# Kernel tuning notes

Hardware: AMD Instinct MI355X
Metric: run time of the kernel (lower is better)

Reference implementation:

```python
import jax, jax.numpy as jnp
import numpy as np

SIZE = 128
WIN = SIZE // 4   # sliding-window size == region size (32)
HALF = WIN // 2   # 16


def _conv(x, w, pad, groups=1):
    return jax.lax.conv_general_dilated(x, w, (1, 1), [(pad, pad), (pad, pad)],
        dimension_numbers=('NCHW', 'OIHW', 'NCHW'), feature_group_count=groups)


def _resize(x, h, w):
    # F.interpolate(..., mode='bilinear', align_corners=False)
    return jax.image.resize(x, (x.shape[0], x.shape[1], h, w), 'bilinear', antialias=False)


def _gauss_kernels():
    ax = np.linspace(-2.0, 2.0, 5)
    xx, yy = np.meshgrid(ax, ax)
    g = np.exp(-(xx ** 2 + yy ** 2) / 2.0) / (2.0 * np.pi)  # sigma = 1
    gx = (-xx * g).astype(np.float32)
    gy = (-yy * g).astype(np.float32)
    return (jnp.asarray(np.tile(gx[None, None], (3, 3, 1, 1))),
            jnp.asarray(np.tile(gy[None, None], (3, 3, 1, 1))))


def _edge_extract(x):
    Gx, Gy = _gauss_kernels()
    h = _conv(x, Gx, 2)
    v = _conv(x, Gy, 2)
    return jnp.tanh(jnp.sqrt(h * h + v * v + 1e-8))


def _color_moments(x, win=5):
    # F.unfold-based local mean / unbiased var / skewness, via depthwise box sums
    C = x.shape[1]
    n = float(win * win)
    ones = jnp.ones((C, 1, win, win), x.dtype)
    box = lambda z: _conv(z, ones, win // 2, groups=C)
    s1 = box(x); s2 = box(x * x); s3 = box(x * x * x)
    mean = s1 / n
    var = (s2 - n * mean * mean) / (n - 1.0)               # unbiased, matches torch.var
    m3 = (s3 - 3.0 * mean * s2 + 2.0 * n * mean ** 3) / n  # E[(x-m)^3]
    skew = m3 / (jnp.sqrt(jnp.maximum(var, 0.0)) ** 3 + 1e-6)
    return jnp.concatenate([mean, var, skew], 1)


def _locate_region(c):
    # scipy: gradient magnitude < 0.2 -> 4-connected label at argmax -> bbox center
    H, W = c.shape
    flat = jnp.argmax(c)
    xm = (flat // W).astype(jnp.int32)
    ym = (flat % W).astype(jnp.int32)
    gm = jnp.hypot(jnp.gradient(c, axis=0), jnp.gradient(c, axis=1))
    mask = gm < 0.2
    seed = jnp.zeros((H, W), bool).at[xm, ym].set(True) & mask

    def dil(r):
        d = r
        d = d | jnp.pad(r[1:, :], ((0, 1), (0, 0)))
        d = d | jnp.pad(r[:-1, :], ((1, 0), (0, 0)))
        d = d | jnp.pad(r[:, 1:], ((0, 0), (0, 1)))
        d = d | jnp.pad(r[:, :-1], ((0, 0), (1, 0)))
        return d & mask

    def body(s):
        r, _ = s
        nr = dil(r)
        return (nr, jnp.any(nr != r))

    region, _ = jax.lax.while_loop(lambda s: s[1], body, (seed, jnp.any(seed)))
    rows = jnp.any(region, 1); cols = jnp.any(region, 0)
    rs = jnp.argmax(rows); re = H - jnp.argmax(rows[::-1])
    cs = jnp.argmax(cols); ce = W - jnp.argmax(cols[::-1])
    ok = mask[xm, ym]  # label_at_max != 0
    x1 = jnp.where(ok, ((rs + re) // 2).astype(jnp.int32), xm)
    y1 = jnp.where(ok, ((cs + ce) // 2).astype(jnp.int32), ym)
    return x1, y1


def _affine_grid(move, H, W):
    # theta = [[1,0,tx],[0,1,ty]] with (tx,ty)=move, align_corners=False
    bx = (2.0 * jnp.arange(W, dtype=jnp.float32) + 1.0) / W - 1.0
    by = (2.0 * jnp.arange(H, dtype=jnp.float32) + 1.0) / H - 1.0
    gx = bx[None, None, :] + move[:, 0, None, None]
    gy = by[None, :, None] + move[:, 1, None, None]
    return jnp.stack(jnp.broadcast_arrays(gx, gy), -1)  # [B,H,W,2]


def _grid_sample(x, grid):
    # bilinear, zeros padding, align_corners=False (torch defaults)
    B, C, H, W = x.shape
    ix = ((grid[..., 0] + 1.0) * W - 1.0) / 2.0
    iy = ((grid[..., 1] + 1.0) * H - 1.0) / 2.0
    ix0 = jnp.floor(ix).astype(jnp.int32)
    iy0 = jnp.floor(iy).astype(jnp.int32)
    wx1 = ix - ix0; wy1 = iy - iy0
    b = jnp.arange(B)[:, None, None]

    def g(yy, xx):
        valid = ((xx >= 0) & (xx < W) & (yy >= 0) & (yy < H)).astype(x.dtype)
        v = x[b, :, jnp.clip(yy, 0, H - 1), jnp.clip(xx, 0, W - 1)]  # [B,Hg,Wg,C]
        return v * valid[..., None]

    out = (g(iy0, ix0) * ((1 - wy1) * (1 - wx1))[..., None]
         + g(iy0, ix0 + 1) * ((1 - wy1) * wx1)[..., None]
         + g(iy0 + 1, ix0) * (wy1 * (1 - wx1))[..., None]
         + g(iy0 + 1, ix0 + 1) * (wy1 * wx1)[..., None])
    return jnp.transpose(out, (0, 3, 1, 2))


def _bn_relu6(x, w, b):
    # BatchNorm2d in training mode (batch stats, biased var, eps=1e-5) + ReLU6
    m = x.mean((0, 2, 3), keepdims=True)
    v = ((x - m) ** 2).mean((0, 2, 3), keepdims=True)
    y = (x - m) / jnp.sqrt(v + 1e-5) * w[None, :, None, None] + b[None, :, None, None]
    return jnp.clip(y, 0.0, 6.0)


def setup_inputs():
    key = jax.random.key(0)
    ks = jax.random.split(key, 8)
    B, C = 8, 64
    return dict(
        warm_flag=1,
        feat1=jax.random.normal(ks[0], (B, C, SIZE, SIZE), jnp.float32),
        feat2=jax.random.normal(ks[1], (B, C, SIZE, SIZE), jnp.float32),
        cam1=jax.random.uniform(ks[2], (B, 64, 64), jnp.float32),
        cam2=jax.random.uniform(ks[3], (B, 64, 64), jnp.float32),
        f_g=jax.random.uniform(ks[4], (B, 3, 512, 512), jnp.float32),
        f_e=jax.random.uniform(ks[5], (B, 3, 512, 512), jnp.float32),
        conv1_w=jax.random.normal(ks[6], (C, 3, 3, 3), jnp.float32) * 0.1,
        conv1_b=jnp.zeros((C,), jnp.float32),
        conv2_w=jax.random.normal(ks[7], (C, 9, 3, 3), jnp.float32) * 0.1,
        conv2_b=jnp.zeros((C,), jnp.float32),
        bn_w=jnp.ones((C,), jnp.float32),
        bn_b=jnp.zeros((C,), jnp.float32),
    )


def reference(warm_flag, feat1, feat2, cam1, cam2, f_g, f_e,
              conv1_w, conv1_b, conv2_w, conv2_b, bn_w, bn_b):
    B = cam1.shape[0]
    c1 = _resize(cam1[:, None], SIZE, SIZE)
    c2 = _resize(cam2[:, None], SIZE, SIZE)

    if warm_flag == 1:
        # numpy/scipy path in torch is detached from autograd
        c1s = jax.lax.stop_gradient(c1)
        c2s = jax.lax.stop_gradient(c2)
        x1, y1 = jax.vmap(_locate_region)(c1s[:, 0])
        # valid-mode box convolution of cam2 with ones((H//4, W//4)), argmax
        box = jax.lax.conv_general_dilated(c2s, jnp.ones((1, 1, WIN, WIN), c2.dtype), (1, 1),
            'VALID', dimension_numbers=('NCHW', 'OIHW', 'NCHW'))[:, 0]
        Wv = box.shape[-1]
        flat = jnp.argmax(box.reshape(B, -1), -1)
        x2 = (flat // Wv + HALF).astype(jnp.int32)
        y2 = (flat % Wv + HALF).astype(jnp.int32)

        idx = jnp.arange(SIZE)
        def rect(xc, yc):
            r = (idx[None, :] >= jnp.maximum(xc - HALF, 0)[:, None]) & \
                (idx[None, :] < jnp.minimum(xc + HALF, SIZE)[:, None])
            cc = (idx[None, :] >= jnp.maximum(yc - HALF, 0)[:, None]) & \
                 (idx[None, :] < jnp.minimum(yc + HALF, SIZE)[:, None])
            return r[:, None, :, None] & cc[:, None, None, :]
        mask1 = rect(x1, y1).astype(feat1.dtype)
        mask2 = rect(x2, y2).astype(feat2.dtype)
        mi1 = jnp.stack([x1, y1], -1).astype(jnp.float32)
        mi2 = jnp.stack([x2, y2], -1).astype(jnp.float32)
    else:
        mask1 = jnp.zeros_like(feat1)
        mask2 = jnp.zeros_like(feat2)
        mi1 = jnp.zeros((B, 2), jnp.float32)
        mi2 = jnp.zeros((B, 2), jnp.float32)

    cam2_move = (mi2 - mi1) / (SIZE // 2)
    cam1_move = (mi1 - mi2) / (SIZE // 2)
    grid1 = _affine_grid(cam1_move, SIZE, SIZE)
    grid2 = _affine_grid(cam2_move, SIZE, SIZE)

    moments = _resize(_color_moments(f_e), SIZE, SIZE)   # [B,9,128,128]
    edge = _resize(_edge_extract(f_g), SIZE, SIZE)       # [B,3,128,128]
    feat1_edge = jnp.clip(_conv(edge, conv1_w, 1) + conv1_b[None, :, None, None], 0.0, 6.0)
    feat2_color = _conv(moments, conv2_w, 1) + conv2_b[None, :, None, None]

    feat2_move = _grid_sample(feat2_color * mask2, grid2)
    feat1_edge_move = _grid_sample(feat1_edge * mask1, grid1)

    Bc, C, H, W = feat1.shape
    f1 = feat1.reshape(Bc, C, -1)
    f2 = feat2.reshape(Bc, C, -1)
    f2m = feat2_move.reshape(Bc, C, -1)
    f1m = feat1_edge_move.reshape(Bc, C, -1)

    f2_attn = jax.nn.softmax(jnp.einsum('bcn,bdn->bcd', f2m, f1), -1)  # [B,C,C]
    feat1_apply = jnp.einsum('bcd,bdn->bcn', f2_attn, f1).reshape(Bc, C, H, W)
    f1_attn = jax.nn.softmax(jnp.einsum('bcn,bdn->bcd', f1m, f2), -1)
    feat2_apply = jnp.einsum('bcd,bdn->bcn', f1_attn, f2).reshape(Bc, C, H, W)

    feat1_apply = _bn_relu6(feat1_apply, bn_w, bn_b)
    feat2_apply = _bn_relu6(feat2_apply, bn_w, bn_b)

    if warm_flag == 0:
        return (feat1, feat2, grid1, grid2, feat1_edge, feat2_color, f1_attn, f2_attn, feat1, feat2)
    return (feat1_apply, feat2_apply, grid1, grid2, feat1_edge, feat2_color, f1_attn, f2_attn, feat1, feat2)
```

## Files before the change

kernel.cpp:

```cpp
#include <hip/hip_runtime.h>
#include <math.h>

#define SIZE 128
#define WIN 32
#define HALF 16
#define B 8
#define C 64
#define N (SIZE*SIZE)
#define BCN 8388608
#define BV 97

#define O_APPLY1   0
#define O_APPLY2   8388608
#define O_GRID1    16777216
#define O_GRID2    17039360
#define O_EDGEF    17301504
#define O_COLORF   25690112
#define O_ATTN1    34078720
#define O_ATTN2    34111488
#define O_FEAT1    34144256
#define O_FEAT2    42532864

#define WS_BNP     0
#define WS_XY      361472
#define WS_MOM     361600
#define WS_EDGE    1541248
#define WS_BN      1737856

#define NEGINF (-3.402823466e+38f)

typedef unsigned __int128 u128;

__device__ __forceinline__ u128 hfill(u128 g, u128 m) {
  u128 p = m;
  g |= p & (g << 1);  p &= p << 1;
  g |= p & (g << 2);  p &= p << 2;
  g |= p & (g << 4);  p &= p << 4;
  g |= p & (g << 8);  p &= p << 8;
  g |= p & (g << 16); p &= p << 16;
  g |= p & (g << 32); p &= p << 32;
  g |= p & (g << 64);
  p = m;
  g |= p & (g >> 1);  p &= p >> 1;
  g |= p & (g >> 2);  p &= p >> 2;
  g |= p & (g >> 4);  p &= p >> 4;
  g |= p & (g >> 8);  p &= p >> 8;
  g |= p & (g >> 16); p &= p >> 16;
  g |= p & (g >> 32); p &= p >> 32;
  g |= p & (g >> 64);
  return g;
}

__global__ __launch_bounds__(256) void k_front(
    const float* __restrict__ cam1, const float* __restrict__ cam2,
    int* __restrict__ xy, float* __restrict__ g1, float* __restrict__ g2) {
  int b = blockIdx.x, tid = threadIdx.x;
  __shared__ float sc[N];
  __shared__ float sc2[N];
  __shared__ float sv[256]; __shared__ int si[256];
  __shared__ unsigned long long mask64[256];
  __shared__ int s_xm, s_ym, s_ok;
  __shared__ int s_x1, s_y1, s_x2, s_y2;

  const float* src1 = cam1 + b * 4096;
  const float* src2 = cam2 + b * 4096;

  float bv = NEGINF; int bi = 0;
  for (int k = 0; k < 64; ++k) {
    int pix = k * 256 + tid;
    int i = pix >> 7, j = pix & 127;
    float fy = fminf(fmaxf(0.5f * (float)i - 0.25f, 0.f), 63.f);
    float fx = fminf(fmaxf(0.5f * (float)j - 0.25f, 0.f), 63.f);
    int y0 = (int)fy; float ty = fy - (float)y0; int y1i = min(y0 + 1, 63);
    int x0 = (int)fx; float tx = fx - (float)x0; int x1i = min(x0 + 1, 63);
    float a00 = src1[y0 * 64 + x0],  a01 = src1[y0 * 64 + x1i];
    float a10 = src1[y1i * 64 + x0], a11 = src1[y1i * 64 + x1i];
    float v1 = (1.f - ty) * ((1.f - tx) * a00 + tx * a01)
             + ty * ((1.f - tx) * a10 + tx * a11);
    float c00 = src2[y0 * 64 + x0],  c01 = src2[y0 * 64 + x1i];
    float c10 = src2[y1i * 64 + x0], c11 = src2[y1i * 64 + x1i];
    float v2 = (1.f - ty) * ((1.f - tx) * c00 + tx * c01)
             + ty * ((1.f - tx) * c10 + tx * c11);
    sc[pix] = v1; sc2[pix] = v2;
    if (v1 > bv) { bv = v1; bi = pix; }
  }
  sv[tid] = bv; si[tid] = bi;
  __syncthreads();
  for (int s = 128; s; s >>= 1) {
    if (tid < s) {
      float ov = sv[tid + s]; int oi = si[tid + s];
      if (ov > sv[tid] || (ov == sv[tid] && oi < si[tid])) { sv[tid] = ov; si[tid] = oi; }
    }
    __syncthreads();
  }
  if (tid == 0) { s_xm = si[0] >> 7; s_ym = si[0] & 127; }
  __syncthreads();

  for (int k = 0; k < 64; ++k) {
    int pix = k * 256 + tid;
    int i = pix >> 7, j = pix & 127;
    float gx_, gy_;
    if (i == 0)        gx_ = sc[128 + j] - sc[j];
    else if (i == 127) gx_ = sc[127 * 128 + j] - sc[126 * 128 + j];
    else               gx_ = 0.5f * (sc[(i + 1) * 128 + j] - sc[(i - 1) * 128 + j]);
    if (j == 0)        gy_ = sc[i * 128 + 1] - sc[i * 128];
    else if (j == 127) gy_ = sc[i * 128 + 127] - sc[i * 128 + 126];
    else               gy_ = 0.5f * (sc[i * 128 + j + 1] - sc[i * 128 + j - 1]);
    bool pred = hypotf(gx_, gy_) < 0.2f;
    unsigned long long bal = __ballot(pred);
    if ((tid & 63) == 0) mask64[(i << 1) + (j >> 6)] = bal;
  }
  __syncthreads();
  if (tid == 0) {
    unsigned long long wdd = mask64[(s_xm << 1) + (s_ym >> 6)];
    s_ok = (int)((wdd >> (s_ym & 63)) & 1ull);
  }
  __syncthreads();

  if (tid < 64) {
    int l = tid;
    u128 m0 = ((u128)mask64[4 * l])     | ((u128)mask64[4 * l + 1] << 64);
    u128 m1 = ((u128)mask64[4 * l + 2]) | ((u128)mask64[4 * l + 3] << 64);
    u128 g0 = 0, g1v = 0;
    if (s_ok && (s_xm >> 1) == l) {
      if ((s_xm & 1) == 0) g0  = ((u128)1) << s_ym;
      else                 g1v = ((u128)1) << s_ym;
    }
    g0  = hfill(g0 & m0, m0);
    g1v = hfill(g1v & m1, m1);
    for (;;) {
      unsigned long long ulo = __shfl_up((unsigned long long)g1v, 1);
      unsigned long long uhi = __shfl_up((unsigned long long)(g1v >> 64), 1);
      u128 up = (l > 0) ? (((u128)ulo) | ((u128)uhi << 64)) : (u128)0;
      unsigned long long dlo = __shfl_down((unsigned long long)g0, 1);
      unsigned long long dhi = __shfl_down((unsigned long long)(g0 >> 64), 1);
      u128 dn = (l < 63) ? (((u128)dlo) | ((u128)dhi << 64)) : (u128)0;
      u128 n0 = hfill((g0 | up | g1v) & m0, m0);
      u128 n1 = hfill((g1v | n0 | dn) & m1, m1);
      bool chg = (n0 != g0) || (n1 != g1v);
      g0 = n0; g1v = n1;
      if (!__any(chg)) break;
    }
    unsigned long long be = __ballot(g0 != 0);
    unsigned long long bo = __ballot(g1v != 0);
    unsigned long long cl = (unsigned long long)(g0 | g1v);
    unsigned long long chh = (unsigned long long)((g0 | g1v) >> 64);
    for (int off = 32; off; off >>= 1) {
      cl  |= __shfl_xor(cl, off);
      chh |= __shfl_xor(chh, off);
    }
    if (l == 0) {
      int rs = 0, re = 0, cs = 0, ce = 0;
      if (be | bo) {
        int af = be ? (__ffsll(be) - 1) : 1000;
        int bf = bo ? (__ffsll(bo) - 1) : 1000;
        rs = min(af * 2, bf * 2 + 1);
        int al = be ? (63 - __clzll(be)) : -1000;
        int bl = bo ? (63 - __clzll(bo)) : -1000;
        re = max(al * 2, bl * 2 + 1) + 1;
        cs = cl ? (__ffsll(cl) - 1) : 64 + (__ffsll(chh) - 1);
        ce = chh ? 128 - __clzll(chh) : 64 - __clzll(cl);
      }
      int x1, y1;
      if (s_ok) { x1 = (rs + re) >> 1; y1 = (cs + ce) >> 1; }
      else      { x1 = s_xm;           y1 = s_ym; }
      xy[b] = x1; xy[8 + b] = y1; s_x1 = x1; s_y1 = y1;
    }
  }
  __syncthreads();

  for (int idx = tid; idx < BV * 128; idx += 256) {
    int rr = idx >> 7, cc = idx & 127;
    float acc = 0.f;
    #pragma unroll
    for (int dy = 0; dy < WIN; ++dy) acc += sc2[(rr + dy) * 128 + cc];
    sc[idx] = acc;
  }
  __syncthreads();

  bv = NEGINF; bi = 0;
  for (int p = tid; p < BV * BV; p += 256) {
    int rr = p / BV, cc = p % BV;
    float s = 0.f;
    #pragma unroll
    for (int dx = 0; dx < WIN; ++dx) s += sc[rr * 128 + cc + dx];
    if (s > bv) { bv = s; bi = p; }
  }
  sv[tid] = bv; si[tid] = bi;
  __syncthreads();
  for (int s = 128; s; s >>= 1) {
    if (tid < s) {
      float ov = sv[tid + s]; int oi = si[tid + s];
      if (ov > sv[tid] || (ov == sv[tid] && oi < si[tid])) { sv[tid] = ov; si[tid] = oi; }
    }
    __syncthreads();
  }
  if (tid == 0) {
    int x2 = si[0] / BV + HALF, y2 = si[0] % BV + HALF;
    xy[16 + b] = x2; xy[24 + b] = y2; s_x2 = x2; s_y2 = y2;
  }
  __syncthreads();

  float x1f = (float)s_x1, y1f = (float)s_y1;
  float x2f = (float)s_x2, y2f = (float)s_y2;
  float m1x = (x1f - x2f) / 64.f, m1y = (y1f - y2f) / 64.f;
  float* g1b = g1 + (size_t)b * N * 2;
  float* g2b = g2 + (size_t)b * N * 2;
  for (int k = 0; k < 64; ++k) {
    int pix = k * 256 + tid;
    int h = pix >> 7, w = pix & 127;
    float bx = (2.f * (float)w + 1.f) / 128.f - 1.f;
    float by = (2.f * (float)h + 1.f) / 128.f - 1.f;
    g1b[pix * 2]     = bx + m1x; g1b[pix * 2 + 1] = by + m1y;
    g2b[pix * 2]     = bx - m1x; g2b[pix * 2 + 1] = by - m1y;
  }
}

__global__ __launch_bounds__(256) void k_prep(const float* __restrict__ fe,
                                              const float* __restrict__ fg,
                                              float* __restrict__ mom,
                                              float* __restrict__ edge) {
  __shared__ float sx[66 * 66];
  int tid = threadIdx.x;
  if (blockIdx.x < 1536) {
    int blk = blockIdx.x;
    int tile = blk & 63, ch = (blk >> 6) % 3, b = blk / 192;
    int ti0 = (tile >> 3) * 16, tj0 = (tile & 7) * 16;
    const float* src = fe + (size_t)(b * 3 + ch) * 262144;
    int oy0 = 4 * ti0 - 1, ox0 = 4 * tj0 - 1;
    for (int l = tid; l < 66 * 66; l += 256) {
      int r = l / 66, cc = l % 66;
      int gy = oy0 + r, gx = ox0 + cc;
      sx[l] = (gy >= 0 && gy < 512 && gx >= 0 && gx < 512) ? src[gy * 512 + gx] : 0.f;
    }
    __syncthreads();
    int ii = tid >> 4, jj = tid & 15;
    int i = ti0 + ii, j = tj0 + jj;
    float s1a[6], s2a[6], s3a[6], s1b[6], s2b[6], s3b[6];
    #pragma unroll
    for (int t = 0; t < 6; ++t) {
      float a1 = 0, a2 = 0, a3 = 0, b1 = 0, b2 = 0, b3 = 0;
      int lx = 4 * jj + t;
      #pragma unroll
      for (int r = 0; r < 6; ++r) {
        float v = sx[(4 * ii + r) * 66 + lx];
        float v2 = v * v, v3 = v2 * v;
        if (r < 5) { a1 += v; a2 += v2; a3 += v3; }
        if (r > 0) { b1 += v; b2 += v2; b3 += v3; }
      }
      s1a[t] = a1; s2a[t] = a2; s3a[t] = a3;
      s1b[t] = b1; s2b[t] = b2; s3b[t] = b3;
    }
    float am = 0, av = 0, as = 0;
    #pragma unroll
    for (int py = 0; py < 2; ++py) {
      #pragma unroll
      for (int px = 0; px < 2; ++px) {
        float s1 = 0, s2 = 0, s3 = 0;
        #pragma unroll
        for (int t = 0; t < 5; ++t) {
          s1 += py ? s1b[px + t] : s1a[px + t];
          s2 += py ? s2b[px + t] : s2a[px + t];
          s3 += py ? s3b[px + t] : s3a[px + t];
        }
        float mean = s1 / 25.f;
        float var  = (s2 - 25.f * mean * mean) / 24.f;
        float m3   = (s3 - 3.f * mean * s2 + 50.f * mean * mean * mean) / 25.f;
        float sq   = sqrtf(fmaxf(var, 0.f));
        float skew = m3 / (sq * sq * sq + 1e-6f);
        am += mean; av += var; as += skew;
      }
    }
    int base = (b * 9 + ch) * N + i * 128 + j;
    mom[base]         = 0.25f * am;
    mom[base + 3 * N] = 0.25f * av;
    mom[base + 6 * N] = 0.25f * as;
  } else {
    int blk = blockIdx.x - 1536;
    int tile = blk & 63, b = blk >> 6;
    int ti0 = (tile >> 3) * 16, tj0 = (tile & 7) * 16;
    const float* s0 = fg + (size_t)b * 3 * 262144;
    int oy0 = 4 * ti0 - 1, ox0 = 4 * tj0 - 1;
    for (int l = tid; l < 66 * 66; l += 256) {
      int r = l / 66, cc = l % 66;
      int gy = oy0 + r, gx = ox0 + cc;
      float v = 0.f;
      if (gy >= 0 && gy < 512 && gx >= 0 && gx < 512) {
        int o = gy * 512 + gx;
        v = s0[o] + s0[262144 + o] + s0[524288 + o];
      }
      sx[l] = v;
    }
    __syncthreads();
    int ii = tid >> 4, jj = tid & 15;
    int i = ti0 + ii, j = tj0 + jj;
    const float INV2PI = 0.15915494309189535f;
    float wg[5], ug[5];
    #pragma unroll
    for (int t = 0; t < 5; ++t) {
      float a = (float)t - 2.f;
      float e = expf(-0.5f * a * a);
      wg[t] = e; ug[t] = -a * e;
    }
    float rAa[6], rAb[6], rBa[6], rBb[6];
    #pragma unroll
    for (int t = 0; t < 6; ++t) {
      float aa = 0, ab = 0, ba = 0, bb = 0;
      int lx = 4 * jj + t;
      #pragma unroll
      for (int r = 0; r < 6; ++r) {
        float v = sx[(4 * ii + r) * 66 + lx];
        if (r < 5) { aa += v * wg[r]; ba += v * ug[r]; }
        if (r > 0) { ab += v * wg[r - 1]; bb += v * ug[r - 1]; }
      }
      rAa[t] = aa; rAb[t] = ab; rBa[t] = ba; rBb[t] = bb;
    }
    float acc = 0.f;
    #pragma unroll
    for (int py = 0; py < 2; ++py) {
      #pragma unroll
      for (int px = 0; px < 2; ++px) {
        float h = 0, v = 0;
        #pragma unroll
        for (int t = 0; t < 5; ++t) {
          float A  = py ? rAb[px + t] : rAa[px + t];
          float Bw = py ? rBb[px + t] : rBa[px + t];
          h += A * ug[t];
          v += Bw * wg[t];
        }
        h *= INV2PI; v *= INV2PI;
        acc += tanhf(sqrtf(h * h + v * v + 1e-8f));
      }
    }
    edge[b * N + i * 128 + j] = 0.25f * acc;
  }
}

__global__ __launch_bounds__(256) void k_conv12(
    const float* __restrict__ edge, const float* __restrict__ w1,
    const float* __restrict__ b1, float* __restrict__ o4,
    const float* __restrict__ mom, const float* __restrict__ w2,
    const float* __restrict__ b2, float* __restrict__ o5) {
  __shared__ float tin[9 * 324];
  __shared__ float wsm[64 * 84];
  int b = blockIdx.x >> 6, tile = blockIdx.x & 63;
  int ti0 = (tile >> 3) * 16, tj0 = (tile & 7) * 16;
  int tid = threadIdx.x;
  int i = tid >> 4, j = tid & 15;
  if (blockIdx.y == 0) {
    for (int l = tid; l < 324; l += 256) {
      int r = l / 18, cc = l % 18;
      int gi = ti0 + r - 1, gj = tj0 + cc - 1;
      tin[l] = (gi >= 0 && gi < 128 && gj >= 0 && gj < 128) ? edge[b * N + gi * 128 + gj] : 0.f;
    }
    for (int l = tid; l < 64 * 12; l += 256) {
      int o = l / 12, t = l % 12;
      wsm[l] = (t < 9) ? (w1[o * 27 + t] + w1[o * 27 + 9 + t] + w1[o * 27 + 18 + t]) : 0.f;
    }
    __syncthreads();
    float win[12];
    #pragma unroll
    for (int dy = 0; dy < 3; ++dy)
      #pragma unroll
      for (int dx = 0; dx < 3; ++dx)
        win[dy * 3 + dx] = tin[(i + dy) * 18 + (j + dx)];
    win[9] = 0.f; win[10] = 0.f; win[11] = 0.f;
    float* o = o4 + (size_t)b * C * N + (ti0 + i) * 128 + tj0 + j;
    for (int oc = 0; oc < C; ++oc) {
      const float4* wr = (const float4*)(wsm + oc * 12);
      float acc = b1[oc];
      #pragma unroll
      for (int q = 0; q < 3; ++q) {
        float4 w4 = wr[q];
        acc += w4.x * win[4 * q] + w4.y * win[4 * q + 1]
             + w4.z * win[4 * q + 2] + w4.w * win[4 * q + 3];
      }
      o[oc * N] = fminf(fmaxf(acc, 0.f), 6.f);
    }
  } else {
    for (int l = tid; l < 9 * 324; l += 256) {
      int ic = l / 324, rem = l % 324, r = rem / 18, cc = rem % 18;
      int gi = ti0 + r - 1, gj = tj0 + cc - 1;
      tin[l] = (gi >= 0 && gi < 128 && gj >= 0 && gj < 128) ? mom[(b * 9 + ic) * N + gi * 128 + gj] : 0.f;
    }
    for (int l = tid; l < 64 * 84; l += 256) {
      int o = l / 84, t = l % 84;
      wsm[l] = (t < 81) ? w2[o * 81 + t] : 0.f;
    }
    __syncthreads();
    float win[84];
    #pragma unroll
    for (int ic = 0; ic < 9; ++ic)
      #pragma unroll
      for (int dy = 0; dy < 3; ++dy)
        #pragma unroll
        for (int dx = 0; dx < 3; ++dx)
          win[ic * 9 + dy * 3 + dx] = tin[ic * 324 + (i + dy) * 18 + (j + dx)];
    win[81] = 0.f; win[82] = 0.f; win[83] = 0.f;
    float* o = o5 + (size_t)b * C * N + (ti0 + i) * 128 + tj0 + j;
    for (int oc = 0; oc < C; ++oc) {
      const float4* wr = (const float4*)(wsm + oc * 84);
      float acc = b2[oc];
      #pragma unroll
      for (int q = 0; q < 21; ++q) {
        float4 w4 = wr[q];
        acc += w4.x * win[4 * q] + w4.y * win[4 * q + 1]
             + w4.z * win[4 * q + 2] + w4.w * win[4 * q + 3];
      }
      o[oc * N] = acc;
    }
  }
}

__global__ __launch_bounds__(256) void k_logits(const float* __restrict__ aB1,
                                                const float* __restrict__ bB1,
                                                const float* __restrict__ aB2,
                                                const float* __restrict__ bB2,
                                                float* __restrict__ lg,
                                                const int* __restrict__ xy) {
  int mode = blockIdx.y;
  const float* aBase = mode ? aB2 : aB1;
  const float* bBase = mode ? bB2 : bB1;
  int b = blockIdx.x >> 4, sl = blockIdx.x & 15;
  int tid = threadIdx.x;
  int ci = (tid >> 4) << 2, di = (tid & 15) << 2;
  float* o = lg + (size_t)(((mode * 8 + b) * 16 + sl)) * 4096;

  int x1 = xy[b], y1 = xy[8 + b], x2 = xy[16 + b], y2 = xy[24 + b];
  int dyh, dxw, rlo, rhi, clo, chi;
  if (mode == 0) {
    dyh = y1 - y2; dxw = x1 - x2;
    rlo = max(x1 - HALF, 0); rhi = min(x1 + HALF, SIZE);
    clo = max(y1 - HALF, 0); chi = min(y1 + HALF, SIZE);
  } else {
    dyh = y2 - y1; dxw = x2 - x1;
    rlo = max(x2 - HALF, 0); rhi = min(x2 + HALF, SIZE);
    clo = max(y2 - HALF, 0); chi = min(y2 + HALF, SIZE);
  }
  int hlo = max(0, rlo - dyh), hhi = min(SIZE, rhi - dyh);
  int wlo = max(0, clo - dxw), whi = min(SIZE, chi - dxw);
  int wn = whi - wlo, hn = hhi - hlo;
  int npos = (wn > 0 && hn > 0) ? wn * hn : 0;
  if (sl * 64 >= npos) {
    #pragma unroll
    for (int u = 0; u < 4; ++u)
      #pragma unroll
      for (int v = 0; v < 4; ++v)
        o[(ci + u) * 64 + (di + v)] = 0.f;
    return;
  }

  __shared__ float aS[64][65];
  __shared__ float bS[64][65];
  const float* aB = aBase + (size_t)b * C * N;
  const float* bB = bBase + (size_t)b * C * N;
  for (int l = tid; l < 4096; l += 256) {
    int ch = l >> 6, k = l & 63;
    int p = sl * 64 + k;
    float av = 0.f, bv = 0.f;
    if (p < npos) {
      int h = hlo + p / wn, w = wlo + p % wn;
      av = aB[ch * N + (h + dyh) * 128 + (w + dxw)];
      bv = bB[ch * N + h * 128 + w];
    }
    aS[ch][k] = av; bS[ch][k] = bv;
  }
  __syncthreads();
  float acc[4][4] = {};
  #pragma unroll 4
  for (int k = 0; k < 64; ++k) {
    float a0 = aS[ci][k], a1 = aS[ci + 1][k], a2 = aS[ci + 2][k], a3 = aS[ci + 3][k];
    float b0 = bS[di][k], b1v = bS[di + 1][k], b2v = bS[di + 2][k], b3 = bS[di + 3][k];
    acc[0][0] += a0 * b0; acc[0][1] += a0 * b1v; acc[0][2] += a0 * b2v; acc[0][3] += a0 * b3;
    acc[1][0] += a1 * b0; acc[1][1] += a1 * b1v; acc[1][2] += a1 * b2v; acc[1][3] += a1 * b3;
    acc[2][0] += a2 * b0; acc[2][1] += a2 * b1v; acc[2][2] += a2 * b2v; acc[2][3] += a2 * b3;
    acc[3][0] += a3 * b0; acc[3][1] += a3 * b1v; acc[3][2] += a3 * b2v; acc[3][3] += a3 * b3;
  }
  #pragma unroll
  for (int u = 0; u < 4; ++u)
    #pragma unroll
    for (int v = 0; v < 4; ++v)
      o[(ci + u) * 64 + (di + v)] = acc[u][v];
}

__global__ void k_softmax(const float* __restrict__ lg,
                          float* __restrict__ o6, float* __restrict__ o7) {
  int row = blockIdx.x;
  int mode = blockIdx.y;
  float* dst = mode ? o7 : o6;
  int b = row >> 6, c = row & 63;
  int lane = threadIdx.x;
  const float* base = lg + (size_t)((mode * 8 + b) * 16) * 4096 + c * 64 + lane;
  float v = 0.f;
  #pragma unroll
  for (int sl = 0; sl < 16; ++sl) v += base[sl * 4096];
  float mx = v;
  for (int off = 32; off; off >>= 1) mx = fmaxf(mx, __shfl_xor(mx, off));
  float e = expf(v - mx);
  float s = e;
  for (int off = 32; off; off >>= 1) s += __shfl_xor(s, off);
  dst[row * 64 + lane] = e / s;
}

__global__ __launch_bounds__(256) void k_applyst(const float* __restrict__ a1,
                                                 const float* __restrict__ s1_,
                                                 float* __restrict__ d1,
                                                 const float* __restrict__ a2,
                                                 const float* __restrict__ s2_,
                                                 float* __restrict__ d2,
                                                 float* __restrict__ bnp) {
  const float* attn; const float* src; float* dst;
  int t = blockIdx.y;
  if (t == 0) { attn = a1; src = s1_; dst = d1; }
  else        { attn = a2; src = s2_; dst = d2; }
  int b = blockIdx.x >> 6, chunk = blockIdx.x & 63;
  int n0 = chunk * 256 + threadIdx.x;
  const float* s = src + (size_t)b * C * N + n0;
  float v[64];
  #pragma unroll
  for (int d = 0; d < 64; ++d) v[d] = s[d * N];
  const float4* at4 = (const float4*)(attn + b * 4096);
  float* o = dst + (size_t)b * C * N + n0;
  __shared__ float red[64][4], red2[64][4];
  int lane = threadIdx.x & 63, wave = threadIdx.x >> 6;
  for (int c = 0; c < 64; ++c) {
    float acc = 0.f;
    #pragma unroll
    for (int q = 0; q < 16; ++q) {
      float4 w4 = at4[c * 16 + q];
      acc += w4.x * v[4 * q] + w4.y * v[4 * q + 1] + w4.z * v[4 * q + 2] + w4.w * v[4 * q + 3];
    }
    o[c * N] = acc;
    float sr = acc, ssr = acc * acc;
    for (int off = 32; off; off >>= 1) {
      sr  += __shfl_xor(sr, off);
      ssr += __shfl_xor(ssr, off);
    }
    if (lane == 0) { red[c][wave] = sr; red2[c][wave] = ssr; }
  }
  __syncthreads();
  if (threadIdx.x < 64) {
    int c = threadIdx.x;
    float sr  = red[c][0] + red[c][1] + red[c][2] + red[c][3];
    float ssr = red2[c][0] + red2[c][1] + red2[c][2] + red2[c][3];
    int idx = (t * 64 + c) * 512 + blockIdx.x;
    bnp[idx]         = sr;
    bnp[65536 + idx] = ssr;
  }
}

__global__ void k_bnstats2(const float* __restrict__ bnp, float* __restrict__ stats) {
  __shared__ float sr[128][4], ssr[128][4];
  int tid = threadIdx.x;
  int combo = tid >> 2, q = tid & 3;
  float s = 0.f, ss = 0.f;
  for (int k = 0; k < 128; ++k) {
    int idx = combo * 512 + q * 128 + k;
    s  += bnp[idx];
    ss += bnp[65536 + idx];
  }
  sr[combo][q] = s; ssr[combo][q] = ss;
  __syncthreads();
  if (q == 0) {
    float S  = sr[combo][0] + sr[combo][1] + sr[combo][2] + sr[combo][3];
    float SS = ssr[combo][0] + ssr[combo][1] + ssr[combo][2] + ssr[combo][3];
    int t = combo >> 6, c = combo & 63;
    float mean = S / 131072.f;
    float var  = SS / 131072.f - mean * mean;
    stats[t * 128 + c]      = mean;
    stats[t * 128 + 64 + c] = 1.f / sqrtf(var + 1e-5f);
  }
}

__global__ __launch_bounds__(256) void k_final(
    const float4* __restrict__ f1, float4* __restrict__ o8,
    const float4* __restrict__ f2, float4* __restrict__ o9,
    float4* __restrict__ o0, float4* __restrict__ o1,
    const float* __restrict__ stats,
    const float* __restrict__ bw, const float* __restrict__ bb) {
  int i = blockIdx.x * 256 + threadIdx.x;
  int t = blockIdx.y;
  if (t == 0) o8[i] = f1[i]; else o9[i] = f2[i];
  float4* p = t ? o1 : o0;
  int c = (i >> 12) & 63;
  float m = stats[t * 128 + c], r = stats[t * 128 + 64 + c];
  float w_ = bw[c], b_ = bb[c];
  float4 v = p[i];
  v.x = fminf(fmaxf((v.x - m) * r * w_ + b_, 0.f), 6.f);
  v.y = fminf(fmaxf((v.y - m) * r * w_ + b_, 0.f), 6.f);
  v.z = fminf(fmaxf((v.z - m) * r * w_ + b_, 0.f), 6.f);
  v.w = fminf(fmaxf((v.w - m) * r * w_ + b_, 0.f), 6.f);
  p[i] = v;
}

extern "C" void kernel_launch(void* const* d_in, const int* in_sizes, int n_in,
                              void* d_out, int out_size, void* d_ws, size_t ws_size,
                              hipStream_t stream) {
  const float* feat1   = (const float*)d_in[1];
  const float* feat2   = (const float*)d_in[2];
  const float* cam1    = (const float*)d_in[3];
  const float* cam2    = (const float*)d_in[4];
  const float* f_g     = (const float*)d_in[5];
  const float* f_e     = (const float*)d_in[6];
  const float* conv1_w = (const float*)d_in[7];
  const float* conv1_b = (const float*)d_in[8];
  const float* conv2_w = (const float*)d_in[9];
  const float* conv2_b = (const float*)d_in[10];
  const float* bn_w    = (const float*)d_in[11];
  const float* bn_b    = (const float*)d_in[12];

  float* out = (float*)d_out;
  float* w = (float*)d_ws;
  int* xy = (int*)(w + WS_XY);

  float* o0 = out + O_APPLY1;
  float* o1 = out + O_APPLY2;
  float* o2 = out + O_GRID1;
  float* o3 = out + O_GRID2;
  float* o4 = out + O_EDGEF;
  float* o5 = out + O_COLORF;
  float* o6 = out + O_ATTN1;
  float* o7 = out + O_ATTN2;
  float* o8 = out + O_FEAT1;
  float* o9 = out + O_FEAT2;

  k_front<<<B, 256, 0, stream>>>(cam1, cam2, xy, o2, o3);

  k_prep<<<2048, 256, 0, stream>>>(f_e, f_g, w + WS_MOM, w + WS_EDGE);

  k_conv12<<<dim3(B * 64, 2), 256, 0, stream>>>(w + WS_EDGE, conv1_w, conv1_b, o4,
                                                w + WS_MOM, conv2_w, conv2_b, o5);

  k_logits<<<dim3(B * 16, 2), 256, 0, stream>>>(o4, feat2, o5, feat1,
                                                w + WS_MOM, xy);

  k_softmax<<<dim3(B * C, 2), 64, 0, stream>>>(w + WS_MOM, o6, o7);

  k_applyst<<<dim3(B * 64, 2), 256, 0, stream>>>(o7, feat1, o0, o6, feat2, o1,
                                                 w + WS_BNP);

  k_bnstats2<<<1, 512, 0, stream>>>(w + WS_BNP, w + WS_BN);

  k_final<<<dim3(BCN / 4 / 256, 2), 256, 0, stream>>>(
      (const float4*)feat1, (float4*)o8, (const float4*)feat2, (float4*)o9,
      (float4*)o0, (float4*)o1, w + WS_BN, bn_w, bn_b);
}
```

Before: 631.5 us.

## Fuse front, prep, and feature copy into one stage kernel

Merges the per-batch region-locating kernel, the moment/edge prep kernel and the feat1/feat2 output copies into a single launch dispatched by block index. The few long-running front blocks can then overlap with the bandwidth-bound prep and copy blocks instead of running alone. The copies are removed from the final BN kernel, which now only normalises in place. All blocks share one large static shared-memory allocation, which can reduce occupancy for the prep and copy blocks.

After: 590.7 us. -6.5%, faster.

```diff
diff --git a/kernel.cpp b/kernel.cpp
--- a/kernel.cpp
+++ b/kernel.cpp
@@ -51,17 +51,153 @@
   return g;
 }
 
-__global__ __launch_bounds__(256) void k_front(
+#define PREP_BASE 8
+#define COPY_BASE 2056
+#define COPY_HALF 8192
+#define STAGE1_GRID (COPY_BASE + 2 * COPY_HALF)
+
+__global__ __launch_bounds__(256) void k_stage1(
     const float* __restrict__ cam1, const float* __restrict__ cam2,
-    int* __restrict__ xy, float* __restrict__ g1, float* __restrict__ g2) {
-  int b = blockIdx.x, tid = threadIdx.x;
-  __shared__ float sc[N];
-  __shared__ float sc2[N];
-  __shared__ float sv[256]; __shared__ int si[256];
-  __shared__ unsigned long long mask64[256];
-  __shared__ int s_xm, s_ym, s_ok;
-  __shared__ int s_x1, s_y1, s_x2, s_y2;
-
+    int* __restrict__ xy, float* __restrict__ g1, float* __restrict__ g2,
+    const float* __restrict__ fe, const float* __restrict__ fg,
+    float* __restrict__ mom, float* __restrict__ edge,
+    const float4* __restrict__ f1, float4* __restrict__ o8,
+    const float4* __restrict__ f2, float4* __restrict__ o9) {
+  __shared__ __align__(16) float smem[33824];
+  int blk = blockIdx.x;
+  int tid = threadIdx.x;
+
+  if (blk >= COPY_BASE) {
+    int c = blk - COPY_BASE;
+    if (c < COPY_HALF) o8[c * 256 + tid] = f1[c * 256 + tid];
+    else { int i = (c - COPY_HALF) * 256 + tid; o9[i] = f2[i]; }
+    return;
+  }
+
+  if (blk >= PREP_BASE) {
+    float* sx = smem;
+    int pblk = blk - PREP_BASE;
+    if (pblk < 1536) {
+      int tile = pblk & 63, ch = (pblk >> 6) % 3, b = pblk / 192;
+      int ti0 = (tile >> 3) * 16, tj0 = (tile & 7) * 16;
+      const float* src = fe + (size_t)(b * 3 + ch) * 262144;
+      int oy0 = 4 * ti0 - 1, ox0 = 4 * tj0 - 1;
+      for (int l = tid; l < 66 * 66; l += 256) {
+        int r = l / 66, cc = l % 66;
+        int gy = oy0 + r, gx = ox0 + cc;
+        sx[l] = (gy >= 0 && gy < 512 && gx >= 0 && gx < 512) ? src[gy * 512 + gx] : 0.f;
+      }
+      __syncthreads();
+      int ii = tid >> 4, jj = tid & 15;
+      int i = ti0 + ii, j = tj0 + jj;
+      float s1a[6], s2a[6], s3a[6], s1b[6], s2b[6], s3b[6];
+      #pragma unroll
+      for (int t = 0; t < 6; ++t) {
+        float a1 = 0, a2 = 0, a3 = 0, b1 = 0, b2 = 0, b3 = 0;
+        int lx = 4 * jj + t;
+        #pragma unroll
+        for (int r = 0; r < 6; ++r) {
+          float v = sx[(4 * ii + r) * 66 + lx];
+          float v2 = v * v, v3 = v2 * v;
+          if (r < 5) { a1 += v; a2 += v2; a3 += v3; }
+          if (r > 0) { b1 += v; b2 += v2; b3 += v3; }
+        }
+        s1a[t] = a1; s2a[t] = a2; s3a[t] = a3;
+        s1b[t] = b1; s2b[t] = b2; s3b[t] = b3;
+      }
+      float am = 0, av = 0, as = 0;
+      #pragma unroll
+      for (int py = 0; py < 2; ++py) {
+        #pragma unroll
+        for (int px = 0; px < 2; ++px) {
+          float s1 = 0, s2 = 0, s3 = 0;
+          #pragma unroll
+          for (int t = 0; t < 5; ++t) {
+            s1 += py ? s1b[px + t] : s1a[px + t];
+            s2 += py ? s2b[px + t] : s2a[px + t];
+            s3 += py ? s3b[px + t] : s3a[px + t];
+          }
+          float mean = s1 / 25.f;
+          float var  = (s2 - 25.f * mean * mean) / 24.f;
+          float m3   = (s3 - 3.f * mean * s2 + 50.f * mean * mean * mean) / 25.f;
+          float sq   = sqrtf(fmaxf(var, 0.f));
+          float skew = m3 / (sq * sq * sq + 1e-6f);
+          am += mean; av += var; as += skew;
+        }
+      }
+      int base = (b * 9 + ch) * N + i * 128 + j;
+      mom[base]         = 0.25f * am;
+      mom[base + 3 * N] = 0.25f * av;
+      mom[base + 6 * N] = 0.25f * as;
+    } else {
+      int eblk = pblk - 1536;
+      int tile = eblk & 63, b = eblk >> 6;
+      int ti0 = (tile >> 3) * 16, tj0 = (tile & 7) * 16;
+      const float* s0 = fg + (size_t)b * 3 * 262144;
+      int oy0 = 4 * ti0 - 1, ox0 = 4 * tj0 - 1;
+      for (int l = tid; l < 66 * 66; l += 256) {
+        int r = l / 66, cc = l % 66;
+        int gy = oy0 + r, gx = ox0 + cc;
+        float v = 0.f;
+        if (gy >= 0 && gy < 512 && gx >= 0 && gx < 512) {
+          int o = gy * 512 + gx;
+          v = s0[o] + s0[262144 + o] + s0[524288 + o];
+        }
+        sx[l] = v;
+      }
+      __syncthreads();
+      int ii = tid >> 4, jj = tid & 15;
+      int i = ti0 + ii, j = tj0 + jj;
+      const float INV2PI = 0.15915494309189535f;
+      float wg[5], ug[5];
+      #pragma unroll
+      for (int t = 0; t < 5; ++t) {
+        float a = (float)t - 2.f;
+        float e = expf(-0.5f * a * a);
+        wg[t] = e; ug[t] = -a * e;
+      }
+      float rAa[6], rAb[6], rBa[6], rBb[6];
+      #pragma unroll
+      for (int t = 0; t < 6; ++t) {
+        float aa = 0, ab = 0, ba = 0, bb = 0;
+        int lx = 4 * jj + t;
+        #pragma unroll
+        for (int r = 0; r < 6; ++r) {
+          float v = sx[(4 * ii + r) * 66 + lx];
+          if (r < 5) { aa += v * wg[r]; ba += v * ug[r]; }
+          if (r > 0) { ab += v * wg[r - 1]; bb += v * ug[r - 1]; }
+        }
+        rAa[t] = aa; rAb[t] = ab; rBa[t] = ba; rBb[t] = bb;
+      }
+      float acc = 0.f;
+      #pragma unroll
+      for (int py = 0; py < 2; ++py) {
+        #pragma unroll
+        for (int px = 0; px < 2; ++px) {
+          float h = 0, v = 0;
+          #pragma unroll
+          for (int t = 0; t < 5; ++t) {
+            float A  = py ? rAb[px + t] : rAa[px + t];
+            float Bw = py ? rBb[px + t] : rBa[px + t];
+            h += A * ug[t];
+            v += Bw * wg[t];
+          }
+          h *= INV2PI; v *= INV2PI;
+          acc += tanhf(sqrtf(h * h + v * v + 1e-8f));
+        }
+      }
+      edge[b * N + i * 128 + j] = 0.25f * acc;
+    }
+    return;
+  }
+
+  float* sc  = smem;
+  float* sc2 = smem + 16384;
+  float* sv  = smem + 32768;
+  int*   si  = (int*)(smem + 33024);
+  unsigned long long* mask64 = (unsigned long long*)(smem + 33280);
+  int* sint = (int*)(smem + 33792);
+  int b = blk;
   const float* src1 = cam1 + b * 4096;
   const float* src2 = cam2 + b * 4096;
 
@@ -93,8 +229,9 @@
     }
     __syncthreads();
   }
-  if (tid == 0) { s_xm = si[0] >> 7; s_ym = si[0] & 127; }
-  __syncthreads();
+  if (tid == 0) { sint[0] = si[0] >> 7; sint[1] = si[0] & 127; }
+  __syncthreads();
+  int s_xm = sint[0], s_ym = sint[1];
 
   for (int k = 0; k < 64; ++k) {
     int pix = k * 256 + tid;
@@ -113,9 +250,10 @@
   __syncthreads();
   if (tid == 0) {
     unsigned long long wdd = mask64[(s_xm << 1) + (s_ym >> 6)];
-    s_ok = (int)((wdd >> (s_ym & 63)) & 1ull);
-  }
-  __syncthreads();
+    sint[2] = (int)((wdd >> (s_ym & 63)) & 1ull);
+  }
+  __syncthreads();
+  int s_ok = sint[2];
 
   if (tid < 64) {
     int l = tid;
@@ -164,7 +302,7 @@
       int x1, y1;
       if (s_ok) { x1 = (rs + re) >> 1; y1 = (cs + ce) >> 1; }
       else      { x1 = s_xm;           y1 = s_ym; }
-      xy[b] = x1; xy[8 + b] = y1; s_x1 = x1; s_y1 = y1;
+      xy[b] = x1; xy[8 + b] = y1; sint[3] = x1; sint[4] = y1;
     }
   }
   __syncthreads();
@@ -197,12 +335,12 @@
   }
   if (tid == 0) {
     int x2 = si[0] / BV + HALF, y2 = si[0] % BV + HALF;
-    xy[16 + b] = x2; xy[24 + b] = y2; s_x2 = x2; s_y2 = y2;
-  }
-  __syncthreads();
-
-  float x1f = (float)s_x1, y1f = (float)s_y1;
-  float x2f = (float)s_x2, y2f = (float)s_y2;
+    xy[16 + b] = x2; xy[24 + b] = y2; sint[5] = x2; sint[6] = y2;
+  }
+  __syncthreads();
+
+  float x1f = (float)sint[3], y1f = (float)sint[4];
+  float x2f = (float)sint[5], y2f = (float)sint[6];
   float m1x = (x1f - x2f) / 64.f, m1y = (y1f - y2f) / 64.f;
   float* g1b = g1 + (size_t)b * N * 2;
   float* g2b = g2 + (size_t)b * N * 2;
@@ -213,126 +351,6 @@
     float by = (2.f * (float)h + 1.f) / 128.f - 1.f;
     g1b[pix * 2]     = bx + m1x; g1b[pix * 2 + 1] = by + m1y;
     g2b[pix * 2]     = bx - m1x; g2b[pix * 2 + 1] = by - m1y;
-  }
-}
-
-__global__ __launch_bounds__(256) void k_prep(const float* __restrict__ fe,
-                                              const float* __restrict__ fg,
-                                              float* __restrict__ mom,
-                                              float* __restrict__ edge) {
-  __shared__ float sx[66 * 66];
-  int tid = threadIdx.x;
-  if (blockIdx.x < 1536) {
-    int blk = blockIdx.x;
-    int tile = blk & 63, ch = (blk >> 6) % 3, b = blk / 192;
-    int ti0 = (tile >> 3) * 16, tj0 = (tile & 7) * 16;
-    const float* src = fe + (size_t)(b * 3 + ch) * 262144;
-    int oy0 = 4 * ti0 - 1, ox0 = 4 * tj0 - 1;
-    for (int l = tid; l < 66 * 66; l += 256) {
-      int r = l / 66, cc = l % 66;
-      int gy = oy0 + r, gx = ox0 + cc;
-      sx[l] = (gy >= 0 && gy < 512 && gx >= 0 && gx < 512) ? src[gy * 512 + gx] : 0.f;
-    }
-    __syncthreads();
-    int ii = tid >> 4, jj = tid & 15;
-    int i = ti0 + ii, j = tj0 + jj;
-    float s1a[6], s2a[6], s3a[6], s1b[6], s2b[6], s3b[6];
-    #pragma unroll
-    for (int t = 0; t < 6; ++t) {
-      float a1 = 0, a2 = 0, a3 = 0, b1 = 0, b2 = 0, b3 = 0;
-      int lx = 4 * jj + t;
-      #pragma unroll
-      for (int r = 0; r < 6; ++r) {
-        float v = sx[(4 * ii + r) * 66 + lx];
-        float v2 = v * v, v3 = v2 * v;
-        if (r < 5) { a1 += v; a2 += v2; a3 += v3; }
-        if (r > 0) { b1 += v; b2 += v2; b3 += v3; }
-      }
-      s1a[t] = a1; s2a[t] = a2; s3a[t] = a3;
-      s1b[t] = b1; s2b[t] = b2; s3b[t] = b3;
-    }
-    float am = 0, av = 0, as = 0;
-    #pragma unroll
-    for (int py = 0; py < 2; ++py) {
-      #pragma unroll
-      for (int px = 0; px < 2; ++px) {
-        float s1 = 0, s2 = 0, s3 = 0;
-        #pragma unroll
-        for (int t = 0; t < 5; ++t) {
-          s1 += py ? s1b[px + t] : s1a[px + t];
-          s2 += py ? s2b[px + t] : s2a[px + t];
-          s3 += py ? s3b[px + t] : s3a[px + t];
-        }
-        float mean = s1 / 25.f;
-        float var  = (s2 - 25.f * mean * mean) / 24.f;
-        float m3   = (s3 - 3.f * mean * s2 + 50.f * mean * mean * mean) / 25.f;
-        float sq   = sqrtf(fmaxf(var, 0.f));
-        float skew = m3 / (sq * sq * sq + 1e-6f);
-        am += mean; av += var; as += skew;
-      }
-    }
-    int base = (b * 9 + ch) * N + i * 128 + j;
-    mom[base]         = 0.25f * am;
-    mom[base + 3 * N] = 0.25f * av;
-    mom[base + 6 * N] = 0.25f * as;
-  } else {
-    int blk = blockIdx.x - 1536;
-    int tile = blk & 63, b = blk >> 6;
-    int ti0 = (tile >> 3) * 16, tj0 = (tile & 7) * 16;
-    const float* s0 = fg + (size_t)b * 3 * 262144;
-    int oy0 = 4 * ti0 - 1, ox0 = 4 * tj0 - 1;
-    for (int l = tid; l < 66 * 66; l += 256) {
-      int r = l / 66, cc = l % 66;
-      int gy = oy0 + r, gx = ox0 + cc;
-      float v = 0.f;
-      if (gy >= 0 && gy < 512 && gx >= 0 && gx < 512) {
-        int o = gy * 512 + gx;
-        v = s0[o] + s0[262144 + o] + s0[524288 + o];
-      }
-      sx[l] = v;
-    }
-    __syncthreads();
-    int ii = tid >> 4, jj = tid & 15;
-    int i = ti0 + ii, j = tj0 + jj;
-    const float INV2PI = 0.15915494309189535f;
-    float wg[5], ug[5];
-    #pragma unroll
-    for (int t = 0; t < 5; ++t) {
-      float a = (float)t - 2.f;
-      float e = expf(-0.5f * a * a);
-      wg[t] = e; ug[t] = -a * e;
-    }
-    float rAa[6], rAb[6], rBa[6], rBb[6];
-    #pragma unroll
-    for (int t = 0; t < 6; ++t) {
-      float aa = 0, ab = 0, ba = 0, bb = 0;
-      int lx = 4 * jj + t;
-      #pragma unroll
-      for (int r = 0; r < 6; ++r) {
-        float v = sx[(4 * ii + r) * 66 + lx];
-        if (r < 5) { aa += v * wg[r]; ba += v * ug[r]; }
-        if (r > 0) { ab += v * wg[r - 1]; bb += v * ug[r - 1]; }
-      }
-      rAa[t] = aa; rAb[t] = ab; rBa[t] = ba; rBb[t] = bb;
-    }
-    float acc = 0.f;
-    #pragma unroll
-    for (int py = 0; py < 2; ++py) {
-      #pragma unroll
-      for (int px = 0; px < 2; ++px) {
-        float h = 0, v = 0;
-        #pragma unroll
-        for (int t = 0; t < 5; ++t) {
-          float A  = py ? rAb[px + t] : rAa[px + t];
-          float Bw = py ? rBb[px + t] : rBa[px + t];
-          h += A * ug[t];
-          v += Bw * wg[t];
-        }
-        h *= INV2PI; v *= INV2PI;
-        acc += tanhf(sqrtf(h * h + v * v + 1e-8f));
-      }
-    }
-    edge[b * N + i * 128 + j] = 0.25f * acc;
   }
 }
 
@@ -572,15 +590,12 @@
   }
 }
 
-__global__ __launch_bounds__(256) void k_final(
-    const float4* __restrict__ f1, float4* __restrict__ o8,
-    const float4* __restrict__ f2, float4* __restrict__ o9,
+__global__ __launch_bounds__(256) void k_bnapply(
     float4* __restrict__ o0, float4* __restrict__ o1,
     const float* __restrict__ stats,
     const float* __restrict__ bw, const float* __restrict__ bb) {
   int i = blockIdx.x * 256 + threadIdx.x;
   int t = blockIdx.y;
-  if (t == 0) o8[i] = f1[i]; else o9[i] = f2[i];
   float4* p = t ? o1 : o0;
   int c = (i >> 12) & 63;
   float m = stats[t * 128 + c], r = stats[t * 128 + 64 + c];
@@ -624,9 +639,10 @@
   float* o8 = out + O_FEAT1;
   float* o9 = out + O_FEAT2;
 
-  k_front<<<B, 256, 0, stream>>>(cam1, cam2, xy, o2, o3);
-
-  k_prep<<<2048, 256, 0, stream>>>(f_e, f_g, w + WS_MOM, w + WS_EDGE);
+  k_stage1<<<STAGE1_GRID, 256, 0, stream>>>(
+      cam1, cam2, xy, o2, o3,
+      f_e, f_g, w + WS_MOM, w + WS_EDGE,
+      (const float4*)feat1, (float4*)o8, (const float4*)feat2, (float4*)o9);
 
   k_conv12<<<dim3(B * 64, 2), 256, 0, stream>>>(w + WS_EDGE, conv1_w, conv1_b, o4,
                                                 w + WS_MOM, conv2_w, conv2_b, o5);
@@ -641,7 +657,6 @@
 
   k_bnstats2<<<1, 512, 0, stream>>>(w + WS_BNP, w + WS_BN);
 
-  k_final<<<dim3(BCN / 4 / 256, 2), 256, 0, stream>>>(
-      (const float4*)feat1, (float4*)o8, (const float4*)feat2, (float4*)o9,
+  k_bnapply<<<dim3(BCN / 4 / 256, 2), 256, 0, stream>>>(
       (float4*)o0, (float4*)o1, w + WS_BN, bn_w, bn_b);
 }
```
